# Kernel tuning notes

Hardware: AMD Instinct MI355X
Metric: run time of the kernel (lower is better)

The kernel has to match this reference:

```python
import jax, jax.numpy as jnp
import numpy as np

# FFM: 20 fields x 500 features each, k=16
NUM_FIELDS = 20
FIELD_SIZE = 500
TOTAL_FEATURES = NUM_FIELDS * FIELD_SIZE  # 10000
K = 16
BATCH = 4096


def setup_inputs() -> dict:
    key = jax.random.key(0)
    kx, kw, kv = jax.random.split(key, 3)
    x = jax.random.uniform(kx, (BATCH, TOTAL_FEATURES), dtype=jnp.float32)
    w = jax.random.normal(kw, (TOTAL_FEATURES, 1), dtype=jnp.float32)
    v = jax.random.normal(kv, (NUM_FIELDS, TOTAL_FEATURES, K), dtype=jnp.float32)
    return {"x": x, "w": w, "v": v}


def reference(x, w, v):
    B = x.shape[0]
    F, S, k = NUM_FIELDS, FIELD_SIZE, K
    # linear term: [B, 1]
    linear = x @ w
    # group features by field (fields are contiguous, equal-sized)
    xr = x.reshape(B, F, S)            # [b, field i, feat within field]
    vr = v.reshape(F, F, S, k)         # [field g (other), field i, feat, k]
    # E[b, g, i, :] = sum over features of field i of x * v[g]
    # i.e. field-i embedding specialized for interaction with field g
    E = jnp.einsum('bis,gisk->bgik', xr, vr)  # [B, F, F, K]
    # pairwise term: sum_{i<j} <E[b, j, i], E[b, i, j]>
    T = jnp.einsum('bjik,bijk->bij', E, E)    # [B, F, F]
    mask = jnp.triu(jnp.ones((F, F), dtype=bool), 1)
    pair = jnp.sum(jnp.where(mask, T, 0.0), axis=(1, 2))[:, None]  # [B, 1]
    return linear + pair
```

## Files before the change

### kernel.cpp

```cpp
#include <hip/hip_runtime.h>
#include <stdint.h>


#define NF 20
#define FS 500
#define TFEAT 10000
#define KD 16
#define NCOL 336
#define NFRG 21
#define KP 512
#define NB 4096
#define ROWE (NF * NCOL)

typedef __bf16 bf16x8 __attribute__((ext_vector_type(8)));
typedef __bf16 bf16x2 __attribute__((ext_vector_type(2)));
typedef float  f32x4  __attribute__((ext_vector_type(4)));
typedef unsigned int u32x4 __attribute__((ext_vector_type(4)));

typedef __attribute__((address_space(1))) const void* as1cv;
typedef __attribute__((address_space(3))) void* as3v;

__device__ inline void gload_lds16(const void* g, void* l) {
  __builtin_amdgcn_global_load_lds((as1cv)g, (as3v)l, 16, 0, 0);
}

__global__ __launch_bounds__(256) void prep_vt(const float* __restrict__ v,
                                               const float* __restrict__ w,
                                               __bf16* __restrict__ VtS) {
  const int i = blockIdx.x / NFRG;
  const int q = blockIdx.x % NFRG;
  const int tdx = threadIdx.x;
  __shared__ float lv[FS * 17];
  if (q < NF) {
    const int k = tdx & 15, sb = tdx >> 4;
    const float* vb = v + ((size_t)q * TFEAT + (size_t)i * FS) * KD;
    for (int it = 0; it < 32; ++it) {
      int s = it * 16 + sb;
      if (s < FS) lv[s * 17 + k] = vb[(size_t)s * KD + k];
    }
    __syncthreads();
  }
  const float* wf = w + (size_t)i * FS;
  __bf16* base = VtS + ((size_t)i * 16 * NFRG + q) * 512;
  for (int it = 0; it < 4; ++it) {
    int p = it * 256 + tdx;
    int t = p >> 6, l = p & 63;
    int r = l >> 2;
    int kk = t * 32 + (((l & 3) ^ ((l >> 3) & 3)) << 3);
    bf16x8 h;
#pragma unroll
    for (int e = 0; e < 8; ++e) {
      int s = kk + e;
      float val = 0.f;
      if (s < FS) {
        if (q < NF) val = lv[s * 17 + r];
        else if (r == 0) val = wf[s];
      }
      h[e] = (__bf16)val;
    }
    *(bf16x8*)(base + (size_t)t * (NFRG * 512) + l * 8) = h;
  }
}

__global__ __launch_bounds__(256, 3) void k1_gemm(
    const float* __restrict__ x, const __bf16* __restrict__ VtS,
    __bf16* __restrict__ E2, int chunk_base, int tiles) {
  __shared__ __bf16 As[2][64][32];
  __shared__ __bf16 Bs[2][NCOL * 32];

  const int bx = blockIdx.x;
  const int i  = bx / tiles;
  const int tb = bx % tiles;
  const int tid = threadIdx.x;
  const int lane = tid & 63, wid = tid >> 6;
  const int b0 = chunk_base + tb * 64;

  const int arow = tid >> 2;
  const int ac8 = (tid & 3) * 8;
  const int apch = (tid & 3) ^ ((tid >> 3) & 3);
  const float* xrow = x + (size_t)(b0 + arow) * TFEAT + i * FS;
  const __bf16* VtSi = VtS + (size_t)i * 16 * NFRG * 512 + lane * 8;

  auto issueB = [&](int t, int buf) {
#pragma unroll
    for (int jj = 0; jj < 6; ++jj) {
      int q = wid + 4 * jj;
      if (q < NFRG)
        gload_lds16(VtSi + ((size_t)t * NFRG + q) * 512,
                    (void*)&Bs[buf][q * 512]);
    }
  };

  f32x4 ar0, ar1;
  auto aload = [&](int t) {
    int kk = t * 32 + ac8;
    int c0 = kk > 496 ? 496 : kk;
    int c1 = kk + 4 > 496 ? 496 : kk + 4;
    ar0 = *(const f32x4*)(xrow + c0);
    ar1 = *(const f32x4*)(xrow + c1);
  };
  auto astore = [&](int buf) {
    bf16x8 h;
    h[0] = (__bf16)ar0[0]; h[1] = (__bf16)ar0[1];
    h[2] = (__bf16)ar0[2]; h[3] = (__bf16)ar0[3];
    h[4] = (__bf16)ar1[0]; h[5] = (__bf16)ar1[1];
    h[6] = (__bf16)ar1[2]; h[7] = (__bf16)ar1[3];
    *(bf16x8*)(&As[buf][arow][apch * 8]) = h;
  };

  const int nfr = wid ? 5 : 6;
  const int Fbase = wid ? (1 + wid * 5) : 0;
  const int ar = lane & 15, akc = lane >> 4;

  f32x4 acc[4][6];
#pragma unroll
  for (int m = 0; m < 4; ++m)
#pragma unroll
    for (int nf = 0; nf < 6; ++nf) acc[m][nf] = (f32x4){0.f, 0.f, 0.f, 0.f};

  aload(0);
  issueB(0, 0);
  astore(0);
  asm volatile("s_waitcnt vmcnt(0) lgkmcnt(0)" ::: "memory");
  __builtin_amdgcn_s_barrier();

  for (int t = 0; t < 16; ++t) {
    const int cur = t & 1;
    if (t < 15) {
      aload(t + 1);
      issueB(t + 1, cur ^ 1);
    }
    __builtin_amdgcn_sched_barrier(0);

    bf16x8 bfr[6];
#pragma unroll
    for (int nf = 0; nf < 6; ++nf)
      if (nf < nfr) {
        int n_ = (Fbase + nf) * 16 + ar;
        int pc = akc ^ ((n_ >> 1) & 3);
        bfr[nf] = *(const bf16x8*)&Bs[cur][n_ * 32 + pc * 8];
      }
#pragma unroll
    for (int m = 0; m < 4; ++m) {
      int row = m * 16 + ar;
      int pch = akc ^ ((row >> 1) & 3);
      bf16x8 af = *(const bf16x8*)(&As[cur][row][pch * 8]);
#pragma unroll
      for (int nf = 0; nf < 6; ++nf)
        if (nf < nfr)
          acc[m][nf] = __builtin_amdgcn_mfma_f32_16x16x32_bf16(af, bfr[nf],
                                                               acc[m][nf], 0, 0, 0);
    }
    if (t < 15) {
      astore(cur ^ 1);
      asm volatile("s_waitcnt vmcnt(0) lgkmcnt(0)" ::: "memory");
      __builtin_amdgcn_s_barrier();
    }
  }

  const int lr4 = akc * 4, lcol = lane & 15;
#pragma unroll
  for (int m = 0; m < 4; ++m)
#pragma unroll
    for (int nf = 0; nf < 6; ++nf)
      if (nf < nfr) {
        int n = (Fbase + nf) * 16 + lcol;
#pragma unroll
        for (int r = 0; r < 4; ++r) {
          int bl = tb * 64 + m * 16 + lr4 + r;
          E2[(size_t)bl * ROWE + i * NCOL + n] = (__bf16)acc[m][nf][r];
        }
      }
}

__global__ __launch_bounds__(256) void k2_pair(
    const __bf16* __restrict__ E2, float* __restrict__ out, int chunk_base) {
  __shared__ __align__(16) unsigned shw[4][3360];
  const int tid = threadIdx.x, lane = tid & 63, wid = tid >> 6;
  const int bl = blockIdx.x * 4 + wid;
  const unsigned* src = (const unsigned*)(E2 + (size_t)bl * ROWE);
  for (int it = 0; it < 14; ++it) {
    int idx = it * 64 + lane;
    if (idx < 840) {
      u32x4 val = *(const u32x4*)(src + (size_t)idx * 4);
      *(u32x4*)&shw[wid][idx * 4] = val;
    }
  }
  __syncthreads();
  const __bf16* sh = (const __bf16*)shw[wid];
  const int k = lane & 15, g = lane >> 4;
  float sum = 0.f;
  for (int i = g; i < NF; i += 4)
    for (int j = i + 1; j < NF; ++j)
      sum += (float)sh[i * NCOL + j * 16 + k] * (float)sh[j * NCOL + i * 16 + k];
  if (lane < NF) sum += (float)sh[lane * NCOL + 320];
#pragma unroll
  for (int off = 32; off; off >>= 1) sum += __shfl_xor(sum, off);
  if (lane == 0) out[chunk_base + bl] = sum;
}

extern "C" void kernel_launch(void* const* d_in, const int* in_sizes, int n_in,
                              void* d_out, int out_size, void* d_ws, size_t ws_size,
                              hipStream_t stream) {
  const float* x = (const float*)d_in[0];
  const float* w = (const float*)d_in[1];
  const float* v = (const float*)d_in[2];
  float* out = (float*)d_out;
  char* ws = (char*)d_ws;

  const size_t vt_bytes = (size_t)NF * 16 * NFRG * 512 * 2;
  __bf16* VtS = (__bf16*)ws;
  __bf16* E2 = (__bf16*)(ws + vt_bytes);

  size_t eavail = (ws_size > vt_bytes) ? ws_size - vt_bytes : 0;
  int Bc = NB;
  while (Bc > 64 && (size_t)Bc * ROWE * 2 > eavail) Bc >>= 1;

  prep_vt<<<NF * NFRG, 256, 0, stream>>>(v, w, VtS);
  for (int cb = 0; cb < NB; cb += Bc) {
    int tiles = Bc / 64;
    k1_gemm<<<NF * tiles, 256, 0, stream>>>(x, VtS, E2, cb, tiles);
    k2_pair<<<Bc / 4, 256, 0, stream>>>(E2, out, cb);
  }
}
```

Baseline: 80.68 us.

## Prefetch A tile two steps ahead and remap workgroups across XCDs

The GEMM kernel now keeps two register sets for the x tile, so global loads for step t+2 are issued while step t computes. The partial s_waitcnt vmcnt(2) lets the barrier proceed without draining the newest A loads, hiding more global latency. The block index is also permuted so consecutive workgroups on the same XCD share the same field i, which should improve L2 reuse of the VtS slices. The cost is extra VGPRs for the second A register set, which could hurt occupancy at launch_bounds(256,3). The code also relies on the order in which the vmcnt counter retires loads, including the asynchronous LDS loads for B.

After: 76.76 us. 4.9% less time.

```diff
diff --git a/kernel.cpp b/kernel.cpp
--- a/kernel.cpp
+++ b/kernel.cpp
@@ -68,9 +68,14 @@
   __shared__ __bf16 As[2][64][32];
   __shared__ __bf16 Bs[2][NCOL * 32];
 
-  const int bx = blockIdx.x;
-  const int i  = bx / tiles;
-  const int tb = bx % tiles;
+  int bid = blockIdx.x;
+  const int nwg = gridDim.x;
+  if ((nwg & 7) == 0) {
+    int cpx = nwg >> 3;
+    bid = (bid & 7) * cpx + (bid >> 3);
+  }
+  const int i  = bid / tiles;
+  const int tb = bid % tiles;
   const int tid = threadIdx.x;
   const int lane = tid & 63, wid = tid >> 6;
   const int b0 = chunk_base + tb * 64;
@@ -91,20 +96,20 @@
     }
   };
 
-  f32x4 ar0, ar1;
-  auto aload = [&](int t) {
+  f32x4 a0A, a1A, a0B, a1B;
+  auto aload = [&](int t, f32x4& r0, f32x4& r1) {
     int kk = t * 32 + ac8;
     int c0 = kk > 496 ? 496 : kk;
     int c1 = kk + 4 > 496 ? 496 : kk + 4;
-    ar0 = *(const f32x4*)(xrow + c0);
-    ar1 = *(const f32x4*)(xrow + c1);
-  };
-  auto astore = [&](int buf) {
+    r0 = *(const f32x4*)(xrow + c0);
+    r1 = *(const f32x4*)(xrow + c1);
+  };
+  auto astore = [&](int buf, const f32x4& r0, const f32x4& r1) {
     bf16x8 h;
-    h[0] = (__bf16)ar0[0]; h[1] = (__bf16)ar0[1];
-    h[2] = (__bf16)ar0[2]; h[3] = (__bf16)ar0[3];
-    h[4] = (__bf16)ar1[0]; h[5] = (__bf16)ar1[1];
-    h[6] = (__bf16)ar1[2]; h[7] = (__bf16)ar1[3];
+    h[0] = (__bf16)r0[0]; h[1] = (__bf16)r0[1];
+    h[2] = (__bf16)r0[2]; h[3] = (__bf16)r0[3];
+    h[4] = (__bf16)r1[0]; h[5] = (__bf16)r1[1];
+    h[6] = (__bf16)r1[2]; h[7] = (__bf16)r1[3];
     *(bf16x8*)(&As[buf][arow][apch * 8]) = h;
   };
 
@@ -118,18 +123,17 @@
 #pragma unroll
     for (int nf = 0; nf < 6; ++nf) acc[m][nf] = (f32x4){0.f, 0.f, 0.f, 0.f};
 
-  aload(0);
+  aload(0, a0A, a1A);
+  astore(0, a0A, a1A);
   issueB(0, 0);
-  astore(0);
-  asm volatile("s_waitcnt vmcnt(0) lgkmcnt(0)" ::: "memory");
+  aload(1, a0B, a1B);
+  asm volatile("s_waitcnt vmcnt(2) lgkmcnt(0)" ::: "memory");
   __builtin_amdgcn_s_barrier();
 
-  for (int t = 0; t < 16; ++t) {
-    const int cur = t & 1;
-    if (t < 15) {
-      aload(t + 1);
-      issueB(t + 1, cur ^ 1);
-    }
+  auto body = [&](int T, int curbuf, f32x4& la0, f32x4& la1,
+                  f32x4& sa0, f32x4& sa1) {
+    if (T < 15) issueB(T + 1, curbuf ^ 1);
+    if (T < 14) aload(T + 2, la0, la1);
     __builtin_amdgcn_sched_barrier(0);
 
     bf16x8 bfr[6];
@@ -138,24 +142,32 @@
       if (nf < nfr) {
         int n_ = (Fbase + nf) * 16 + ar;
         int pc = akc ^ ((n_ >> 1) & 3);
-        bfr[nf] = *(const bf16x8*)&Bs[cur][n_ * 32 + pc * 8];
+        bfr[nf] = *(const bf16x8*)&Bs[curbuf][n_ * 32 + pc * 8];
       }
 #pragma unroll
     for (int m = 0; m < 4; ++m) {
       int row = m * 16 + ar;
       int pch = akc ^ ((row >> 1) & 3);
-      bf16x8 af = *(const bf16x8*)(&As[cur][row][pch * 8]);
+      bf16x8 af = *(const bf16x8*)(&As[curbuf][row][pch * 8]);
 #pragma unroll
       for (int nf = 0; nf < 6; ++nf)
         if (nf < nfr)
           acc[m][nf] = __builtin_amdgcn_mfma_f32_16x16x32_bf16(af, bfr[nf],
                                                                acc[m][nf], 0, 0, 0);
     }
-    if (t < 15) {
-      astore(cur ^ 1);
-      asm volatile("s_waitcnt vmcnt(0) lgkmcnt(0)" ::: "memory");
+    if (T < 15) {
+      astore(curbuf ^ 1, sa0, sa1);
+      if (T < 14)
+        asm volatile("s_waitcnt vmcnt(2) lgkmcnt(0)" ::: "memory");
+      else
+        asm volatile("s_waitcnt vmcnt(0) lgkmcnt(0)" ::: "memory");
       __builtin_amdgcn_s_barrier();
     }
+  };
+
+  for (int tt = 0; tt < 16; tt += 2) {
+    body(tt,     0, a0A, a1A, a0B, a1B);
+    body(tt + 1, 1, a0B, a1B, a0A, a1A);
   }
 
   const int lr4 = akc * 4, lcol = lane & 15;
```

## Process two K-slices per iteration and remap blocks for L2 locality

Applied to the files above, without the earlier changes.

The GEMM main loop now consumes 64 K-elements per iteration by treating the two LDS buffers as two K-subtiles, which halves the number of barrier/wait rounds. The cost is that the B prefetch for the next step is only issued after compute and an extra barrier, so B loads no longer overlap compute. A-loads are widened to 16 floats per thread. Block IDs are also remapped in groups of 8 so that neighbouring workgroups land on the same XCD, aiming at better L2 reuse of the shared VtS slices.

Result: faster. 72.60 us (-10.0%).

```diff
diff --git a/kernel.cpp b/kernel.cpp
--- a/kernel.cpp
+++ b/kernel.cpp
@@ -68,44 +68,57 @@
   __shared__ __bf16 As[2][64][32];
   __shared__ __bf16 Bs[2][NCOL * 32];
 
-  const int bx = blockIdx.x;
-  const int i  = bx / tiles;
-  const int tb = bx % tiles;
+  int bid = blockIdx.x;
+  const int nwg = gridDim.x;
+  if ((nwg & 7) == 0) {
+    int cpx = nwg >> 3;
+    bid = (bid & 7) * cpx + (bid >> 3);
+  }
+  const int i  = bid / tiles;
+  const int tb = bid % tiles;
   const int tid = threadIdx.x;
   const int lane = tid & 63, wid = tid >> 6;
   const int b0 = chunk_base + tb * 64;
 
   const int arow = tid >> 2;
-  const int ac8 = (tid & 3) * 8;
-  const int apch = (tid & 3) ^ ((tid >> 3) & 3);
+  const int ac16 = (tid & 3) * 16;
+  const int ah  = (tid & 3) >> 1;
+  const int gh0 = (2 * (tid & 3)) & 3;
+  const int rsw = (arow >> 1) & 3;
   const float* xrow = x + (size_t)(b0 + arow) * TFEAT + i * FS;
   const __bf16* VtSi = VtS + (size_t)i * 16 * NFRG * 512 + lane * 8;
 
-  auto issueB = [&](int t, int buf) {
+  auto issueB = [&](int t) {
 #pragma unroll
     for (int jj = 0; jj < 6; ++jj) {
       int q = wid + 4 * jj;
-      if (q < NFRG)
-        gload_lds16(VtSi + ((size_t)t * NFRG + q) * 512,
-                    (void*)&Bs[buf][q * 512]);
+      if (q < NFRG) {
+        gload_lds16(VtSi + ((size_t)(2 * t) * NFRG + q) * 512,
+                    (void*)&Bs[0][q * 512]);
+        gload_lds16(VtSi + ((size_t)(2 * t + 1) * NFRG + q) * 512,
+                    (void*)&Bs[1][q * 512]);
+      }
     }
   };
 
-  f32x4 ar0, ar1;
+  f32x4 ar_[4];
   auto aload = [&](int t) {
-    int kk = t * 32 + ac8;
-    int c0 = kk > 496 ? 496 : kk;
-    int c1 = kk + 4 > 496 ? 496 : kk + 4;
-    ar0 = *(const f32x4*)(xrow + c0);
-    ar1 = *(const f32x4*)(xrow + c1);
+#pragma unroll
+    for (int j = 0; j < 4; ++j) {
+      int c = t * 64 + ac16 + j * 4;
+      if (c > 496) c = 496;
+      ar_[j] = *(const f32x4*)(xrow + c);
+    }
   };
-  auto astore = [&](int buf) {
-    bf16x8 h;
-    h[0] = (__bf16)ar0[0]; h[1] = (__bf16)ar0[1];
-    h[2] = (__bf16)ar0[2]; h[3] = (__bf16)ar0[3];
-    h[4] = (__bf16)ar1[0]; h[5] = (__bf16)ar1[1];
-    h[6] = (__bf16)ar1[2]; h[7] = (__bf16)ar1[3];
-    *(bf16x8*)(&As[buf][arow][apch * 8]) = h;
+  auto astore = [&]() {
+    bf16x8 h0, h1;
+#pragma unroll
+    for (int e = 0; e < 4; ++e) {
+      h0[e] = (__bf16)ar_[0][e]; h0[4 + e] = (__bf16)ar_[1][e];
+      h1[e] = (__bf16)ar_[2][e]; h1[4 + e] = (__bf16)ar_[3][e];
+    }
+    *(bf16x8*)(&As[ah][arow][((gh0)     ^ rsw) * 8]) = h0;
+    *(bf16x8*)(&As[ah][arow][((gh0 + 1) ^ rsw) * 8]) = h1;
   };
 
   const int nfr = wid ? 5 : 6;
@@ -119,40 +132,40 @@
     for (int nf = 0; nf < 6; ++nf) acc[m][nf] = (f32x4){0.f, 0.f, 0.f, 0.f};
 
   aload(0);
-  issueB(0, 0);
-  astore(0);
+  issueB(0);
+  astore();
   asm volatile("s_waitcnt vmcnt(0) lgkmcnt(0)" ::: "memory");
   __builtin_amdgcn_s_barrier();
 
-  for (int t = 0; t < 16; ++t) {
-    const int cur = t & 1;
-    if (t < 15) {
-      aload(t + 1);
-      issueB(t + 1, cur ^ 1);
-    }
+  for (int t = 0; t < 8; ++t) {
+    if (t < 7) aload(t + 1);
     __builtin_amdgcn_sched_barrier(0);
 
-    bf16x8 bfr[6];
-#pragma unroll
-    for (int nf = 0; nf < 6; ++nf)
-      if (nf < nfr) {
-        int n_ = (Fbase + nf) * 16 + ar;
-        int pc = akc ^ ((n_ >> 1) & 3);
-        bfr[nf] = *(const bf16x8*)&Bs[cur][n_ * 32 + pc * 8];
-      }
-#pragma unroll
-    for (int m = 0; m < 4; ++m) {
-      int row = m * 16 + ar;
-      int pch = akc ^ ((row >> 1) & 3);
-      bf16x8 af = *(const bf16x8*)(&As[cur][row][pch * 8]);
+#pragma unroll
+    for (int ks = 0; ks < 2; ++ks) {
+      bf16x8 af[4];
+#pragma unroll
+      for (int m = 0; m < 4; ++m) {
+        int row = m * 16 + ar;
+        int pch = akc ^ ((row >> 1) & 3);
+        af[m] = *(const bf16x8*)(&As[ks][row][pch * 8]);
+      }
 #pragma unroll
       for (int nf = 0; nf < 6; ++nf)
-        if (nf < nfr)
-          acc[m][nf] = __builtin_amdgcn_mfma_f32_16x16x32_bf16(af, bfr[nf],
-                                                               acc[m][nf], 0, 0, 0);
-    }
-    if (t < 15) {
-      astore(cur ^ 1);
+        if (nf < nfr) {
+          int n_ = (Fbase + nf) * 16 + ar;
+          int pc = akc ^ ((n_ >> 1) & 3);
+          bf16x8 bfr = *(const bf16x8*)&Bs[ks][n_ * 32 + pc * 8];
+#pragma unroll
+          for (int m = 0; m < 4; ++m)
+            acc[m][nf] = __builtin_amdgcn_mfma_f32_16x16x32_bf16(af[m], bfr,
+                                                                 acc[m][nf], 0, 0, 0);
+        }
+    }
+    if (t < 7) {
+      __builtin_amdgcn_s_barrier();
+      issueB(t + 1);
+      astore();
       asm volatile("s_waitcnt vmcnt(0) lgkmcnt(0)" ::: "memory");
       __builtin_amdgcn_s_barrier();
     }
```
